# Kernel optimization log

Hardware: AMD Instinct MI355X
Metric: run time of the kernel (lower is better)

Reference implementation:

```python
import jax, jax.numpy as jnp
import numpy as np

N_NODES = 100000
N_EDGES = 1600000
IN_DIM = 128
OUT_DIM = 128
ORDER = 2
EPS = 1e-9


def setup_inputs() -> dict:
    key = jax.random.key(0)
    ks = jax.random.split(key, 4)
    features = jax.random.normal(ks[0], (N_NODES, IN_DIM), dtype=jnp.float32)
    src = jax.random.randint(ks[1], (N_EDGES,), 0, N_NODES)
    dst = jax.random.randint(ks[2], (N_EDGES,), 0, N_NODES)
    w = jnp.ones((N_EDGES,), dtype=jnp.float32)
    D_norm = jax.random.uniform(ks[3], (N_NODES, 1), dtype=jnp.float32)
    # xavier-normal-ish init for the order+1 linear weights
    Wk = jax.random.split(jax.random.key(1), ORDER + 1)
    std = np.sqrt(2.0 / (IN_DIM + OUT_DIM)).astype(np.float32)
    W = jnp.stack([jax.random.normal(k, (OUT_DIM, IN_DIM), dtype=jnp.float32) * std for k in Wk])
    b = jnp.zeros((ORDER + 1, OUT_DIM), dtype=jnp.float32)
    scale = jnp.ones((ORDER + 1, OUT_DIM), dtype=jnp.float32)
    offset = jnp.zeros((ORDER + 1, OUT_DIM), dtype=jnp.float32)
    return {"features": features, "src": src, "dst": dst, "w": w,
            "D_norm": D_norm, "W": W, "b": b, "scale": scale, "offset": offset}


def reference(features, src, dst, w, D_norm, W, b, scale, offset):
    N = features.shape[0]

    def feat_trans(ft, i):
        h = ft @ W[i].T + b[i]          # [N, out]
        h = jax.nn.relu(h)
        mean = jnp.mean(h, axis=1, keepdims=True)
        var = jnp.var(h, axis=1, keepdims=True) + EPS  # unbiased=False
        return (h - mean) * scale[i] * jax.lax.rsqrt(var) + offset[i]

    h_hop = [features]
    for _ in range(ORDER):
        m = h_hop[-1][src] * w[:, None]                 # u_mul_e gather  [E, d]
        agg = jax.ops.segment_sum(m, dst, num_segments=N)  # sum reduce to dst
        h_hop.append(agg * D_norm)

    h_part = [feat_trans(ft, i) for i, ft in enumerate(h_hop)]
    return jnp.concatenate(h_part, axis=1)  # aggr='concat' -> [N, (order+1)*out]
```

## Files before the change

kernel.cpp:

```cpp
#include <hip/hip_runtime.h>
#include <hip/hip_bf16.h>

#define OUT_STRIDE 384
#define EPSV 1e-9f
#define BSH 10
#define BS 1024
#define NBMAX 512
#define CH 4096

typedef __attribute__((ext_vector_type(8))) short bf16x8;
typedef __attribute__((ext_vector_type(4))) float f32x4;

static __device__ __forceinline__ unsigned short f2bf(float f) {
    __hip_bfloat16 h = __float2bfloat16(f);
    return *reinterpret_cast<unsigned short*>(&h);
}

__global__ __launch_bounds__(256)
void multisplit_pack_kernel(const int* __restrict__ src, const int* __restrict__ dst,
                            const float* __restrict__ w, int* __restrict__ bcur,
                            int* __restrict__ rec, int E, int CAP,
                            const float* __restrict__ features,
                            unsigned short* __restrict__ featb, long n4) {
    __shared__ int hist[NBMAX], scan_[NBMAX], gbase[NBMAX], lcur[NBMAX];
    __shared__ int recS[CH * 3];
    __shared__ int wt[4];
    const int t = threadIdx.x;
    const int lane = t & 63, wv = t >> 6;
    const int c0 = blockIdx.x * CH;
    const int cnt_total = min(CH, E - c0);

    for (int i = t; i < NBMAX; i += 256) hist[i] = 0;
    __syncthreads();
    #pragma unroll
    for (int p = 0; p < CH / 256; ++p) {
        int i = c0 + p * 256 + t;
        if (i < E) atomicAdd(&hist[dst[i] >> BSH], 1);
    }
    __syncthreads();
    {
        int b0 = 2 * t, b1 = 2 * t + 1;
        int h0 = hist[b0], h1 = hist[b1];
        int s = h0 + h1;
        int inc = s;
        #pragma unroll
        for (int d = 1; d < 64; d <<= 1) { int u = __shfl_up(inc, d); if (lane >= d) inc += u; }
        if (lane == 63) wt[wv] = inc;
        __syncthreads();
        int base = 0;
        for (int w2 = 0; w2 < wv; ++w2) base += wt[w2];
        int ex = base + inc - s;
        scan_[b0] = ex;
        scan_[b1] = ex + h0;
    }
    __syncthreads();
    for (int i = t; i < NBMAX; i += 256) {
        if (hist[i] > 0) gbase[i] = atomicAdd(&bcur[i], hist[i]);
        lcur[i] = scan_[i];
    }
    __syncthreads();
    #pragma unroll
    for (int p = 0; p < CH / 256; ++p) {
        int i = c0 + p * 256 + t;
        if (i < E) {
            int d = dst[i];
            int b = d >> BSH;
            int j = atomicAdd(&lcur[b], 1);
            recS[3 * j]     = src[i];
            recS[3 * j + 1] = d;
            recS[3 * j + 2] = __float_as_int(w[i]);
        }
    }
    __syncthreads();
    #pragma unroll
    for (int p = 0; p < CH / 256; ++p) {
        int j = p * 256 + t;
        if (j < cnt_total) {
            int d = recS[3 * j + 1];
            int b = d >> BSH;
            int g = gbase[b] + (j - scan_[b]);
            if (g < CAP) {
                long gp = (long)b * CAP + g;
                rec[3 * gp]     = recS[3 * j];
                rec[3 * gp + 1] = d;
                rec[3 * gp + 2] = recS[3 * j + 2];
            }
        }
    }
    long gid = blockIdx.x * blockDim.x + threadIdx.x;
    long stride = (long)gridDim.x * blockDim.x;
    for (long p = gid; p < n4; p += stride) {
        float4 v = ((const float4*)features)[p];
        ushort4 o;
        o.x = f2bf(v.x); o.y = f2bf(v.y); o.z = f2bf(v.z); o.w = f2bf(v.w);
        *(ushort4*)&featb[p * 4] = o;
    }
}

__global__ __launch_bounds__(256)
void bucket_csr_kernel(const int* __restrict__ rec, const int* __restrict__ bcur,
                       int* __restrict__ off, int* __restrict__ deg,
                       int2* __restrict__ ed, int N, int CAP) {
    __shared__ int h[BS];
    __shared__ int wt[4];
    const int b = blockIdx.x;
    const int t = threadIdx.x;
    const int lane = t & 63, wv = t >> 6;
    const int cnt = min(bcur[b], CAP);
    const long base = (long)b * CAP;
    const int n0 = b << BSH;
    const int nn = min(BS, N - n0);

    for (int i = t; i < BS; i += 256) h[i] = 0;
    __syncthreads();
    for (int i = t; i < cnt; i += 256) atomicAdd(&h[rec[3 * (base + i) + 1] - n0], 1);
    __syncthreads();
    {
        int j0 = 4 * t;
        int l0 = h[j0], l1 = h[j0 + 1], l2 = h[j0 + 2], l3 = h[j0 + 3];
        int s = l0 + l1 + l2 + l3;
        int inc = s;
        #pragma unroll
        for (int d = 1; d < 64; d <<= 1) { int u = __shfl_up(inc, d); if (lane >= d) inc += u; }
        if (lane == 63) wt[wv] = inc;
        __syncthreads();
        int base_ = 0;
        for (int w2 = 0; w2 < wv; ++w2) base_ += wt[w2];
        int ex = base_ + inc - s;
        int e_[4] = {ex, ex + l0, ex + l0 + l1, ex + l0 + l1 + l2};
        int c_[4] = {l0, l1, l2, l3};
        __syncthreads();
        #pragma unroll
        for (int k = 0; k < 4; ++k) {
            h[j0 + k] = e_[k];
            if (j0 + k < nn) {
                off[n0 + j0 + k] = (int)(base + e_[k]);
                deg[n0 + j0 + k] = c_[k];
            }
        }
    }
    __syncthreads();
    for (int i = t; i < cnt; i += 256) {
        int d = rec[3 * (base + i) + 1] - n0;
        int pos = atomicAdd(&h[d], 1);
        ed[base + pos] = make_int2(rec[3 * (base + i)], rec[3 * (base + i) + 2]);
    }
}

__device__ __forceinline__ void acc8(float* a, int4 r, float w) {
    #pragma unroll
    for (int j = 0; j < 4; ++j) {
        int bits = (&r.x)[j];
        float f0 = __int_as_float(bits << 16);
        float f1 = __int_as_float(bits & 0xffff0000);
        a[2 * j]     += f0 * w;
        a[2 * j + 1] += f1 * w;
    }
}

__global__ __launch_bounds__(256)
void gather_wave(const unsigned short* __restrict__ X,
                 const int* __restrict__ off, const int* __restrict__ deg,
                 const int2* __restrict__ ed,
                 const float* __restrict__ Dn,
                 unsigned short* __restrict__ outb, int N) {
    const int tid = threadIdx.x;
    const int n = blockIdx.x * 4 + (tid >> 6);
    if (n >= N) return;
    const int lane = tid & 63;
    const int g2 = lane >> 4;
    const int l = lane & 15;
    const int beg = off[n];
    const int end = beg + deg[n];
    float a[8] = {0.f, 0.f, 0.f, 0.f, 0.f, 0.f, 0.f, 0.f};
    const unsigned short* Xc = X + 8 * l;
    int i = beg + g2;
    for (; i + 12 < end; i += 16) {
        int2 e0 = ed[i], e1 = ed[i + 4], e2 = ed[i + 8], e3 = ed[i + 12];
        int4 r0 = *(const int4*)(Xc + (long)e0.x * 128);
        int4 r1 = *(const int4*)(Xc + (long)e1.x * 128);
        int4 r2 = *(const int4*)(Xc + (long)e2.x * 128);
        int4 r3 = *(const int4*)(Xc + (long)e3.x * 128);
        acc8(a, r0, __int_as_float(e0.y));
        acc8(a, r1, __int_as_float(e1.y));
        acc8(a, r2, __int_as_float(e2.y));
        acc8(a, r3, __int_as_float(e3.y));
    }
    for (; i < end; i += 4) {
        int2 e0 = ed[i];
        int4 r0 = *(const int4*)(Xc + (long)e0.x * 128);
        acc8(a, r0, __int_as_float(e0.y));
    }
    #pragma unroll
    for (int j = 0; j < 8; ++j) {
        a[j] += __shfl_xor(a[j], 16);
        a[j] += __shfl_xor(a[j], 32);
    }
    if (g2 == 0) {
        const float dn = Dn[n];
        int4 o;
        #pragma unroll
        for (int j = 0; j < 4; ++j) {
            unsigned lo = f2bf(a[2 * j] * dn);
            unsigned hi = f2bf(a[2 * j + 1] * dn);
            (&o.x)[j] = (int)((hi << 16) | lo);
        }
        *(int4*)&outb[(long)n * 128 + 8 * l] = o;
    }
}

#define XS 136

__device__ __forceinline__ void stage_W(const float* __restrict__ Wf_hop, short* Wl, int tid) {
    const float4* W4 = (const float4*)Wf_hop;
    for (int idx = tid; idx < 128 * 32; idx += 256) {
        float4 v = W4[idx];
        int row = idx >> 5;
        int col = (idx & 31) * 4;
        short* p = &Wl[row * XS + col];
        p[0] = f2bf(v.x); p[1] = f2bf(v.y); p[2] = f2bf(v.z); p[3] = f2bf(v.w);
    }
}

__device__ __forceinline__ void mfma_ln_epilogue(
    const short* Xl, const short* Wl,
    const float* __restrict__ bp, const float* __restrict__ sp, const float* __restrict__ op,
    float* out, int ocol, int n0, int N, int tid)
{
    const int lane = tid & 63;
    const int wv = tid >> 6;
    f32x4 acc[8];
    #pragma unroll
    for (int c = 0; c < 8; ++c) acc[c] = (f32x4){0.f, 0.f, 0.f, 0.f};
    const int rsub = lane & 15;
    const int g = lane >> 4;
    const short* xbase = &Xl[(wv * 16 + rsub) * XS + g * 8];
    const short* wbase = &Wl[rsub * XS + g * 8];
    #pragma unroll
    for (int kk = 0; kk < 4; ++kk) {
        bf16x8 a = *(const bf16x8*)(xbase + kk * 32);
        #pragma unroll
        for (int c = 0; c < 8; ++c) {
            bf16x8 bb = *(const bf16x8*)(wbase + c * 16 * XS + kk * 32);
            acc[c] = __builtin_amdgcn_mfma_f32_16x16x32_bf16(a, bb, acc[c], 0, 0, 0);
        }
    }
    float sum[4] = {0.f, 0.f, 0.f, 0.f};
    float ssq[4] = {0.f, 0.f, 0.f, 0.f};
    #pragma unroll
    for (int c = 0; c < 8; ++c) {
        float bias = bp[c * 16 + rsub];
        #pragma unroll
        for (int r = 0; r < 4; ++r) {
            float h = acc[c][r] + bias;
            h = fmaxf(h, 0.0f);
            acc[c][r] = h;
            sum[r] += h;
            ssq[r] += h * h;
        }
    }
    #pragma unroll
    for (int msk = 1; msk < 16; msk <<= 1) {
        #pragma unroll
        for (int r = 0; r < 4; ++r) {
            sum[r] += __shfl_xor(sum[r], msk);
            ssq[r] += __shfl_xor(ssq[r], msk);
        }
    }
    #pragma unroll
    for (int r = 0; r < 4; ++r) {
        int n = n0 + wv * 16 + g * 4 + r;
        if (n >= N) continue;
        float mean = sum[r] * (1.0f / 128.0f);
        float var = ssq[r] * (1.0f / 128.0f) - mean * mean + EPSV;
        float inv = rsqrtf(var);
        float* orow = out + (long)n * OUT_STRIDE + ocol;
        #pragma unroll
        for (int c = 0; c < 8; ++c) {
            int col = c * 16 + rsub;
            orow[col] = (acc[c][r] - mean) * sp[col] * inv + op[col];
        }
    }
}

__global__ __launch_bounds__(256)
void transform3_kernel(const unsigned short* __restrict__ featb,
                       const unsigned short* __restrict__ h1b,
                       const unsigned short* __restrict__ h2b,
                       const float* __restrict__ Wf,
                       const float* __restrict__ bf, const float* __restrict__ scf,
                       const float* __restrict__ offp,
                       float* out, int N)
{
    const int hop = blockIdx.y;
    const int tid = threadIdx.x;
    __shared__ __attribute__((aligned(16))) short Wl[128 * XS];
    __shared__ __attribute__((aligned(16))) short Xl[64 * XS];
    stage_W(Wf + (long)hop * 128 * 128, Wl, tid);
    const unsigned short* xb = (hop == 0) ? featb : (hop == 1) ? h1b : h2b;
    const int n0 = blockIdx.x * 64;
    for (int idx = tid; idx < 64 * 16; idx += 256) {
        int r = idx >> 4;
        int c = (idx & 15) * 8;
        int n = n0 + r;
        int4 v = make_int4(0, 0, 0, 0);
        if (n < N) v = *(const int4*)(xb + (long)n * 128 + c);
        *(int4*)&Xl[r * XS + c] = v;
    }
    __syncthreads();
    mfma_ln_epilogue(Xl, Wl, bf + hop * 128, scf + hop * 128, offp + hop * 128,
                     out, hop * 128, n0, N, tid);
}

__global__ __launch_bounds__(256)
void scatter_kernel(const float* X, long xstride, long xcol0,
                    const int* __restrict__ src, const int* __restrict__ dst,
                    const float* __restrict__ w, const float* __restrict__ Dn,
                    int useDn, float* out, long ocol0, int nE)
{
    const int lane = threadIdx.x & 63;
    const int wave = (int)((blockIdx.x * blockDim.x + threadIdx.x) >> 6);
    const int nWaves = (int)((gridDim.x * blockDim.x) >> 6);
    for (int e = wave; e < nE; e += nWaves) {
        const int s = src[e];
        const int d = dst[e];
        float ww = w[e];
        if (useDn) ww *= Dn[s];
        const float2 v = *(const float2*)(X + (long)s * xstride + xcol0 + 2 * lane);
        float* o = out + (long)d * OUT_STRIDE + ocol0 + 2 * lane;
        atomicAdd(o, v.x * ww);
        atomicAdd(o + 1, v.y * ww);
    }
}

__global__ __launch_bounds__(256)
void transform_f32_kernel(const float* x, long xs, int useDnIn,
                          const float* __restrict__ Dn,
                          const float* __restrict__ Wf_hop,
                          const float* __restrict__ bp, const float* __restrict__ sp,
                          const float* __restrict__ op,
                          float* out, int ocol, int N)
{
    __shared__ __attribute__((aligned(16))) short Wl[128 * XS];
    __shared__ __attribute__((aligned(16))) short Xl[64 * XS];
    const int tid = threadIdx.x;
    stage_W(Wf_hop, Wl, tid);
    const int n0 = blockIdx.x * 64;
    for (int idx = tid; idx < 64 * 32; idx += 256) {
        int r = idx >> 5;
        int col = (idx & 31) * 4;
        int n = n0 + r;
        float4 v = make_float4(0.f, 0.f, 0.f, 0.f);
        float m = 1.0f;
        if (n < N) {
            v = *(const float4*)(x + (long)n * xs + col);
            if (useDnIn) m = Dn[n];
        }
        short* p = &Xl[r * XS + col];
        p[0] = f2bf(v.x * m); p[1] = f2bf(v.y * m); p[2] = f2bf(v.z * m); p[3] = f2bf(v.w * m);
    }
    __syncthreads();
    mfma_ln_epilogue(Xl, Wl, bp, sp, op, out, ocol, n0, N, tid);
}

extern "C" void kernel_launch(void* const* d_in, const int* in_sizes, int n_in,
                              void* d_out, int out_size, void* d_ws, size_t ws_size,
                              hipStream_t stream) {
    const float* features = (const float*)d_in[0];
    const int*   src      = (const int*)d_in[1];
    const int*   dst      = (const int*)d_in[2];
    const float* w        = (const float*)d_in[3];
    const float* Dn       = (const float*)d_in[4];
    const float* W        = (const float*)d_in[5];
    const float* b        = (const float*)d_in[6];
    const float* scale    = (const float*)d_in[7];
    const float* offset   = (const float*)d_in[8];
    float* out = (float*)d_out;
    const int N = in_sizes[0] / 128;
    const int E = in_sizes[1];
    const int NB = (N + BS - 1) >> BSH;
    const int nblk = (N + 63) / 64;
    int CAP = ((E / (NB > 0 ? NB : 1)) * 3 / 2 + 255) & ~255;
    if (CAP < 1024) CAP = 1024;

    const size_t o_off = 0;
    const size_t o_deg = (size_t)N;
    const size_t o_ed  = ((size_t)2 * N + 3) & ~(size_t)3;
    const size_t o_bc  = o_ed + 2 * (size_t)NB * CAP;
    const size_t o_rec = (o_bc + NB + 3) & ~(size_t)3;
    const size_t o_fb  = o_rec + 3 * (size_t)NB * CAP;
    const size_t need  = (o_fb + 3 * (size_t)64 * N) * 4;

    if (NB <= NBMAX && ws_size >= need) {
        int* ws_i  = (int*)d_ws;
        int* off   = ws_i + o_off;
        int* deg   = ws_i + o_deg;
        int2* ed   = (int2*)(ws_i + o_ed);
        int* bcur  = ws_i + o_bc;
        int* rec   = ws_i + o_rec;
        unsigned short* featb = (unsigned short*)(ws_i + o_fb);
        unsigned short* h1b   = featb + (size_t)N * 128;
        unsigned short* h2b   = h1b + (size_t)N * 128;

        hipMemsetAsync(bcur, 0, (size_t)NB * 4, stream);
        multisplit_pack_kernel<<<(E + CH - 1) / CH, 256, 0, stream>>>(
            src, dst, w, bcur, rec, E, CAP, features, featb, (long)N * 32);
        bucket_csr_kernel<<<NB, 256, 0, stream>>>(rec, bcur, off, deg, ed, N, CAP);

        gather_wave<<<(N + 3) / 4, 256, 0, stream>>>(featb, off, deg, ed, Dn, h1b, N);
        gather_wave<<<(N + 3) / 4, 256, 0, stream>>>(h1b, off, deg, ed, Dn, h2b, N);

        dim3 tg(nblk, 3);
        transform3_kernel<<<tg, 256, 0, stream>>>(featb, h1b, h2b, W, b, scale, offset, out, N);
    } else {
        hipMemsetAsync(out, 0, (size_t)out_size * sizeof(float), stream);
        scatter_kernel<<<2048, 256, 0, stream>>>(features, 128, 0, src, dst, w, Dn, 0, out, 128, E);
        scatter_kernel<<<2048, 256, 0, stream>>>(out, OUT_STRIDE, 128, src, dst, w, Dn, 1, out, 256, E);
        transform_f32_kernel<<<nblk, 256, 0, stream>>>(features, 128, 0, Dn, W, b, scale, offset, out, 0, N);
        transform_f32_kernel<<<nblk, 256, 0, stream>>>(out + 128, OUT_STRIDE, 1, Dn, W + 128 * 128, b + 128, scale + 128, offset + 128, out, 128, N);
        transform_f32_kernel<<<nblk, 256, 0, stream>>>(out + 256, OUT_STRIDE, 1, Dn, W + 2 * 128 * 128, b + 256, scale + 256, offset + 256, out, 256, N);
    }
}
```

Before: 349.9 us.

## Split edge records into SoA, halve bucket size, process two tiles per transform block

```diff
diff --git a/kernel.cpp b/kernel.cpp
--- a/kernel.cpp
+++ b/kernel.cpp
@@ -3,8 +3,8 @@
 
 #define OUT_STRIDE 384
 #define EPSV 1e-9f
-#define BSH 10
-#define BS 1024
+#define BSH 9
+#define BS 512
 #define NBMAX 512
 #define CH 4096
 
@@ -19,7 +19,7 @@
 __global__ __launch_bounds__(256)
 void multisplit_pack_kernel(const int* __restrict__ src, const int* __restrict__ dst,
                             const float* __restrict__ w, int* __restrict__ bcur,
-                            int* __restrict__ rec, int E, int CAP,
+                            int2* __restrict__ edw, int* __restrict__ dl, int E, int CAP,
                             const float* __restrict__ features,
                             unsigned short* __restrict__ featb, long n4) {
     __shared__ int hist[NBMAX], scan_[NBMAX], gbase[NBMAX], lcur[NBMAX];
@@ -81,9 +81,8 @@
             int g = gbase[b] + (j - scan_[b]);
             if (g < CAP) {
                 long gp = (long)b * CAP + g;
-                rec[3 * gp]     = recS[3 * j];
-                rec[3 * gp + 1] = d;
-                rec[3 * gp + 2] = recS[3 * j + 2];
+                edw[gp] = make_int2(recS[3 * j], recS[3 * j + 2]);
+                dl[gp]  = d;
             }
         }
     }
@@ -98,7 +97,8 @@
 }
 
 __global__ __launch_bounds__(256)
-void bucket_csr_kernel(const int* __restrict__ rec, const int* __restrict__ bcur,
+void bucket_csr_kernel(const int2* __restrict__ edw, const int* __restrict__ dl,
+                       const int* __restrict__ bcur,
                        int* __restrict__ off, int* __restrict__ deg,
                        int2* __restrict__ ed, int N, int CAP) {
     __shared__ int h[BS];
@@ -113,12 +113,12 @@
 
     for (int i = t; i < BS; i += 256) h[i] = 0;
     __syncthreads();
-    for (int i = t; i < cnt; i += 256) atomicAdd(&h[rec[3 * (base + i) + 1] - n0], 1);
+    for (int i = t; i < cnt; i += 256) atomicAdd(&h[dl[base + i] - n0], 1);
     __syncthreads();
     {
-        int j0 = 4 * t;
-        int l0 = h[j0], l1 = h[j0 + 1], l2 = h[j0 + 2], l3 = h[j0 + 3];
-        int s = l0 + l1 + l2 + l3;
+        int j0 = 2 * t;
+        int l0 = h[j0], l1 = h[j0 + 1];
+        int s = l0 + l1;
         int inc = s;
         #pragma unroll
         for (int d = 1; d < 64; d <<= 1) { int u = __shfl_up(inc, d); if (lane >= d) inc += u; }
@@ -127,23 +127,17 @@
         int base_ = 0;
         for (int w2 = 0; w2 < wv; ++w2) base_ += wt[w2];
         int ex = base_ + inc - s;
-        int e_[4] = {ex, ex + l0, ex + l0 + l1, ex + l0 + l1 + l2};
-        int c_[4] = {l0, l1, l2, l3};
+        int e0 = ex, e1 = ex + l0;
         __syncthreads();
-        #pragma unroll
-        for (int k = 0; k < 4; ++k) {
-            h[j0 + k] = e_[k];
-            if (j0 + k < nn) {
-                off[n0 + j0 + k] = (int)(base + e_[k]);
-                deg[n0 + j0 + k] = c_[k];
-            }
-        }
+        h[j0] = e0; h[j0 + 1] = e1;
+        if (j0 < nn)     { off[n0 + j0]     = (int)(base + e0); deg[n0 + j0]     = l0; }
+        if (j0 + 1 < nn) { off[n0 + j0 + 1] = (int)(base + e1); deg[n0 + j0 + 1] = l1; }
     }
     __syncthreads();
     for (int i = t; i < cnt; i += 256) {
-        int d = rec[3 * (base + i) + 1] - n0;
+        int d = dl[base + i] - n0;
         int pos = atomicAdd(&h[d], 1);
-        ed[base + pos] = make_int2(rec[3 * (base + i)], rec[3 * (base + i) + 2]);
+        ed[base + pos] = edw[base + i];
     }
 }
 
@@ -298,18 +292,22 @@
     __shared__ __attribute__((aligned(16))) short Xl[64 * XS];
     stage_W(Wf + (long)hop * 128 * 128, Wl, tid);
     const unsigned short* xb = (hop == 0) ? featb : (hop == 1) ? h1b : h2b;
-    const int n0 = blockIdx.x * 64;
-    for (int idx = tid; idx < 64 * 16; idx += 256) {
-        int r = idx >> 4;
-        int c = (idx & 15) * 8;
-        int n = n0 + r;
-        int4 v = make_int4(0, 0, 0, 0);
-        if (n < N) v = *(const int4*)(xb + (long)n * 128 + c);
-        *(int4*)&Xl[r * XS + c] = v;
-    }
-    __syncthreads();
-    mfma_ln_epilogue(Xl, Wl, bf + hop * 128, scf + hop * 128, offp + hop * 128,
-                     out, hop * 128, n0, N, tid);
+    #pragma unroll
+    for (int t2 = 0; t2 < 2; ++t2) {
+        const int n0 = (blockIdx.x * 2 + t2) * 64;
+        for (int idx = tid; idx < 64 * 16; idx += 256) {
+            int r = idx >> 4;
+            int c = (idx & 15) * 8;
+            int n = n0 + r;
+            int4 v = make_int4(0, 0, 0, 0);
+            if (n < N) v = *(const int4*)(xb + (long)n * 128 + c);
+            *(int4*)&Xl[r * XS + c] = v;
+        }
+        __syncthreads();
+        mfma_ln_epilogue(Xl, Wl, bf + hop * 128, scf + hop * 128, offp + hop * 128,
+                         out, hop * 128, n0, N, tid);
+        __syncthreads();
+    }
 }
 
 __global__ __launch_bounds__(256)
@@ -382,13 +380,15 @@
     const int nblk = (N + 63) / 64;
     int CAP = ((E / (NB > 0 ? NB : 1)) * 3 / 2 + 255) & ~255;
     if (CAP < 1024) CAP = 1024;
+    const size_t NC = (size_t)NB * CAP;
 
     const size_t o_off = 0;
     const size_t o_deg = (size_t)N;
     const size_t o_ed  = ((size_t)2 * N + 3) & ~(size_t)3;
-    const size_t o_bc  = o_ed + 2 * (size_t)NB * CAP;
-    const size_t o_rec = (o_bc + NB + 3) & ~(size_t)3;
-    const size_t o_fb  = o_rec + 3 * (size_t)NB * CAP;
+    const size_t o_bc  = o_ed + 2 * NC;
+    const size_t o_un  = (o_bc + NB + 3) & ~(size_t)3;
+    const size_t o_dl  = o_un + 2 * NC;
+    const size_t o_fb  = o_dl + NC;
     const size_t need  = (o_fb + 3 * (size_t)64 * N) * 4;
 
     if (NB <= NBMAX && ws_size >= need) {
@@ -397,20 +397,21 @@
         int* deg   = ws_i + o_deg;
         int2* ed   = (int2*)(ws_i + o_ed);
         int* bcur  = ws_i + o_bc;
-        int* rec   = ws_i + o_rec;
+        int2* edw  = (int2*)(ws_i + o_un);
+        int* dl    = ws_i + o_dl;
         unsigned short* featb = (unsigned short*)(ws_i + o_fb);
         unsigned short* h1b   = featb + (size_t)N * 128;
         unsigned short* h2b   = h1b + (size_t)N * 128;
 
         hipMemsetAsync(bcur, 0, (size_t)NB * 4, stream);
         multisplit_pack_kernel<<<(E + CH - 1) / CH, 256, 0, stream>>>(
-            src, dst, w, bcur, rec, E, CAP, features, featb, (long)N * 32);
-        bucket_csr_kernel<<<NB, 256, 0, stream>>>(rec, bcur, off, deg, ed, N, CAP);
+            src, dst, w, bcur, edw, dl, E, CAP, features, featb, (long)N * 32);
+        bucket_csr_kernel<<<NB, 256, 0, stream>>>(edw, dl, bcur, off, deg, ed, N, CAP);
 
         gather_wave<<<(N + 3) / 4, 256, 0, stream>>>(featb, off, deg, ed, Dn, h1b, N);
         gather_wave<<<(N + 3) / 4, 256, 0, stream>>>(h1b, off, deg, ed, Dn, h2b, N);
 
-        dim3 tg(nblk, 3);
+        dim3 tg((N + 127) / 128, 3);
         transform3_kernel<<<tg, 256, 0, stream>>>(featb, h1b, h2b, W, b, scale, offset, out, N);
     } else {
         hipMemsetAsync(out, 0, (size_t)out_size * sizeof(float), stream);
```

Measured after the change: 323.0 us. 1.08x faster.
